# Optimization experiments

Hardware: AMD Instinct MI355X
Metric: run time of the kernel (lower is better)

## Reference

```python
import jax, jax.numpy as jnp
import numpy as np

N = 100000
E = 3200000
EMBED = 64
RBF = 16
EPS_ANGLE = 1e-8
EPS_NORM = 1e-12  # F.normalize default eps


def _linear(h, W, b):
    return h @ W + b


def setup_inputs() -> dict:
    key = jax.random.key(0)
    ks = jax.random.split(key, 12)
    s = lambda fan_in: 1.0 / np.sqrt(fan_in)
    return {
        "x": jax.random.normal(ks[0], (N, EMBED), jnp.float32),
        "coord": jax.random.normal(ks[1], (N, 3), jnp.float32),
        "rbf_feature": jax.random.normal(ks[2], (E, RBF), jnp.float32),
        "edge_index": jax.random.randint(ks[3], (2, E), 0, N, jnp.int64),
        # edge_mlp: Linear(RBF+1, EMBED) -> SiLU -> Linear(EMBED, EMBED)
        "W1": jax.random.uniform(ks[4], (RBF + 1, EMBED), jnp.float32, -s(RBF + 1), s(RBF + 1)),
        "b1": jnp.zeros((EMBED,), jnp.float32),
        "W2": jax.random.uniform(ks[5], (EMBED, EMBED), jnp.float32, -s(EMBED), s(EMBED)),
        "b2": jnp.zeros((EMBED,), jnp.float32),
        # update_mlp: Linear(EMBED, EMBED) -> SiLU -> Linear(EMBED, EMBED)
        "W3": jax.random.uniform(ks[6], (EMBED, EMBED), jnp.float32, -s(EMBED), s(EMBED)),
        "b3": jnp.zeros((EMBED,), jnp.float32),
        "W4": jax.random.uniform(ks[7], (EMBED, EMBED), jnp.float32, -s(EMBED), s(EMBED)),
        "b4": jnp.zeros((EMBED,), jnp.float32),
    }


def reference(x, coord, rbf_feature, edge_index, W1, b1, W2, b2, W3, b3, W4, b4):
    row, col = edge_index[0], edge_index[1]
    # gather per-edge displacement vectors: [E, 3]
    v = coord[row] - coord[col]
    # compute_angle(v, -v): normalize both, cosine, clamp, acos
    norm = jnp.maximum(jnp.linalg.norm(v, axis=-1, keepdims=True), EPS_NORM)
    vn = v / norm
    cos_angle = jnp.clip(jnp.sum(vn * (-vn), axis=-1), -1.0 + EPS_ANGLE, 1.0 - EPS_ANGLE)
    angle = jnp.arccos(cos_angle)[:, None]  # [E, 1]
    edge_feat = jnp.concatenate([rbf_feature, angle], axis=-1)  # [E, RBF+1]
    # edge MLP
    edge_msg = _linear(jax.nn.silu(_linear(edge_feat, W1, b1)), W2, b2)  # [E, EMBED]
    # scatter-add to source nodes (index_add_ over row)
    agg = jax.ops.segment_sum(edge_msg, row, num_segments=x.shape[0])  # [N, EMBED]
    # node update
    return x + _linear(jax.nn.silu(_linear(agg, W3, b3)), W4, b4)
```

## Files before the change

### kernel.cpp

```cpp
#include <hip/hip_runtime.h>
#include <hip/hip_fp16.h>

typedef __attribute__((ext_vector_type(8))) short bf16x8;
typedef __attribute__((ext_vector_type(4))) float f32x4;

constexpr int EMBED = 64;
constexpr int RBF   = 16;
constexpr int EPB   = 256;
constexpr int EPW   = 64;

__device__ __forceinline__ short f2bf(float f) {
    unsigned u = __float_as_uint(f);
    unsigned r = (u + 0x7fffu + ((u >> 16) & 1u)) >> 16;
    return (short)(r & 0xffffu);
}

__device__ __forceinline__ unsigned pk_f16(float lo, float hi) {
    __half2 h = __halves2half2(__float2half_rn(lo), __float2half_rn(hi));
    return *reinterpret_cast<unsigned*>(&h);
}

__device__ __forceinline__ void atom_pk_add_f16(__half* addr, unsigned data) {
    asm volatile("global_atomic_pk_add_f16 %0, %1, off"
                 :: "v"(addr), "v"(data) : "memory");
}

__device__ __forceinline__ int ch_map(int t, int c) {
    return (t & 1) + 2 * c + 32 * (t >> 1);
}

template <bool USE_F16>
__global__ __launch_bounds__(256, 2) void edge_kernel(
    const float* __restrict__ coord,
    const float* __restrict__ rbf,
    const int* __restrict__ edge_index,
    const float* __restrict__ W1,
    const float* __restrict__ b1,
    const float* __restrict__ W2,
    const float* __restrict__ b2,
    void* __restrict__ aggv,
    long long E)
{
    __shared__ int lds_row[EPB];
    __shared__ __align__(16) short lds_s[4][4][16 * 64];

    const int tid  = threadIdx.x;
    const int lane = tid & 63;
    const int wave = tid >> 6;
    const int g = lane >> 4;
    const int c = lane & 15;
    const long long blk_e0 = (long long)blockIdx.x * EPB;

    {
        long long e = blk_e0 + tid;
        lds_row[tid] = (e < E) ? edge_index[e] : 0;
    }
    __builtin_amdgcn_wave_barrier();

    bf16x8 b1f[4];
#pragma unroll
    for (int t = 0; t < 4; ++t) {
#pragma unroll
        for (int j = 0; j < 8; ++j) {
            const int k = g * 8 + j;
            const int n = t * 16 + c;
            b1f[t][j] = (k <= RBF) ? f2bf(W1[k * EMBED + n]) : (short)0;
        }
    }
    bf16x8 b2f[2][4];
#pragma unroll
    for (int kk = 0; kk < 2; ++kk)
#pragma unroll
        for (int t = 0; t < 4; ++t) {
            const int ch = ch_map(t, c);
#pragma unroll
            for (int j = 0; j < 8; ++j) {
                const int k = kk * 32 + g * 8 + j;
                b2f[kk][t][j] = f2bf(W2[k * EMBED + ch]);
            }
        }
    float b1v[4], b2v[4];
#pragma unroll
    for (int t = 0; t < 4; ++t) {
        b1v[t] = b1[t * 16 + c];
        b2v[t] = b2[ch_map(t, c)];
    }

    const long long wave_e0 = blk_e0 + (long long)wave * EPW;

    bf16x8 a1[4];
#pragma unroll
    for (int mt = 0; mt < 4; ++mt) {
        bf16x8 a = {};
        const long long e0 = wave_e0 + mt * 16;
        const int eloc0 = wave * EPW + mt * 16;
        const long long ea = e0 + c;
        const bool ev = (ea < E);
        if (g < 2) {
            if (ev) {
                const float4 p0 = *reinterpret_cast<const float4*>(rbf + ea * RBF + g * 8);
                const float4 p1 = *reinterpret_cast<const float4*>(rbf + ea * RBF + g * 8 + 4);
                a[0] = f2bf(p0.x); a[1] = f2bf(p0.y); a[2] = f2bf(p0.z); a[3] = f2bf(p0.w);
                a[4] = f2bf(p1.x); a[5] = f2bf(p1.y); a[6] = f2bf(p1.z); a[7] = f2bf(p1.w);
            }
        } else if (g == 2) {
            if (ev) {
                const int row = lds_row[eloc0 + c];
                const int col = edge_index[E + ea];
                const float vx = coord[row * 3 + 0] - coord[col * 3 + 0];
                const float vy = coord[row * 3 + 1] - coord[col * 3 + 1];
                const float vz = coord[row * 3 + 2] - coord[col * 3 + 2];
                const float sq = vx * vx + vy * vy + vz * vz;
                const float nrm = fmaxf(sqrtf(sq), 1e-12f);
                const float inv = 1.0f / nrm;
                const float ux = vx * inv, uy = vy * inv, uz = vz * inv;
                const float s2 = ux * ux + uy * uy + uz * uz;
                const float cosang = fminf(fmaxf(-s2, -1.0f), 1.0f);
                const float ang = acosf(cosang);
                a[0] = f2bf(ang);
            }
        }
        a1[mt] = a;
    }

#pragma unroll
    for (int mt = 0; mt < 4; ++mt) {
        f32x4 acc1[4];
#pragma unroll
        for (int t = 0; t < 4; ++t) {
            f32x4 ci = {b1v[t], b1v[t], b1v[t], b1v[t]};
            acc1[t] = __builtin_amdgcn_mfma_f32_16x16x32_bf16(a1[mt], b1f[t], ci, 0, 0, 0);
        }
        char* const sl = reinterpret_cast<char*>(lds_s[wave][mt]);
#pragma unroll
        for (int t = 0; t < 4; ++t)
#pragma unroll
            for (int r = 0; r < 4; ++r) {
                const float x = acc1[t][r];
                const float s = x / (1.0f + __expf(-x));
                const int erow = g * 4 + r;
                const int byte = erow * 128 + ((t * 32 + 2 * c) ^ ((erow & 7) << 4));
                *reinterpret_cast<short*>(sl + byte) = f2bf(s);
            }
    }
    __builtin_amdgcn_wave_barrier();

#pragma unroll
    for (int mt = 0; mt < 4; ++mt) {
        const long long e0 = wave_e0 + mt * 16;
        const int eloc0 = wave * EPW + mt * 16;
        const char* const sl = reinterpret_cast<const char*>(lds_s[wave][mt]);

        bf16x8 a2[2];
#pragma unroll
        for (int kk = 0; kk < 2; ++kk) {
            const int byte = c * 128 + ((kk * 64 + g * 16) ^ ((c & 7) << 4));
            a2[kk] = *reinterpret_cast<const bf16x8*>(sl + byte);
        }

        f32x4 acc2[4];
#pragma unroll
        for (int t = 0; t < 4; ++t) {
            f32x4 ci = {b2v[t], b2v[t], b2v[t], b2v[t]};
            acc2[t] = __builtin_amdgcn_mfma_f32_16x16x32_bf16(a2[0], b2f[0][t], ci, 0, 0, 0);
            acc2[t] = __builtin_amdgcn_mfma_f32_16x16x32_bf16(a2[1], b2f[1][t], acc2[t], 0, 0, 0);
        }

#pragma unroll
        for (int r = 0; r < 4; ++r) {
            const long long eat = e0 + g * 4 + r;
            if (eat < E) {
                const long long rowoff = (long long)lds_row[eloc0 + g * 4 + r] * EMBED;
                if (USE_F16) {
                    __half* const dst = reinterpret_cast<__half*>(aggv) + rowoff;
                    atom_pk_add_f16(dst + 2 * c,      pk_f16(acc2[0][r], acc2[1][r]));
                    atom_pk_add_f16(dst + 32 + 2 * c, pk_f16(acc2[2][r], acc2[3][r]));
                } else {
                    float* const dst = reinterpret_cast<float*>(aggv) + rowoff;
                    atomicAdd(dst + 2 * c,      acc2[0][r]);
                    atomicAdd(dst + 2 * c + 1,  acc2[1][r]);
                    atomicAdd(dst + 32 + 2 * c, acc2[2][r]);
                    atomicAdd(dst + 33 + 2 * c, acc2[3][r]);
                }
            }
        }
    }
}

template <bool USE_F16>
__global__ __launch_bounds__(256) void node_kernel(
    const float* __restrict__ x,
    const void* __restrict__ aggv,
    const float* __restrict__ W3,
    const float* __restrict__ b3,
    const float* __restrict__ W4,
    const float* __restrict__ b4,
    float* __restrict__ out,
    int nn)
{
    __shared__ __align__(16) float lds_s[4][EMBED];
    const int lane = threadIdx.x & 63;
    const int wave = threadIdx.x >> 6;

    float w3c[EMBED], w4c[EMBED];
#pragma unroll
    for (int j = 0; j < EMBED; ++j) w3c[j] = W3[j * EMBED + lane];
#pragma unroll
    for (int j = 0; j < EMBED; ++j) w4c[j] = W4[j * EMBED + lane];
    const float b3v = b3[lane];
    const float b4v = b4[lane];

    const float4* s4 = reinterpret_cast<const float4*>(lds_s[wave]);

    const int wid = blockIdx.x * 4 + wave;
    const int nw  = gridDim.x * 4;
    for (int n = wid; n < nn; n += nw) {
        const long long base = (long long)n * EMBED + lane;
        float a;
        if (USE_F16) {
            a = __half2float(reinterpret_cast<const __half*>(aggv)[base]);
        } else {
            a = reinterpret_cast<const float*>(aggv)[base];
        }

        lds_s[wave][lane] = a;
        __builtin_amdgcn_wave_barrier();

        float acc = b3v;
#pragma unroll
        for (int j4 = 0; j4 < EMBED / 4; ++j4) {
            const float4 sv = s4[j4];
            acc = fmaf(sv.x, w3c[4 * j4 + 0], acc);
            acc = fmaf(sv.y, w3c[4 * j4 + 1], acc);
            acc = fmaf(sv.z, w3c[4 * j4 + 2], acc);
            acc = fmaf(sv.w, w3c[4 * j4 + 3], acc);
        }
        const float s = acc / (1.0f + __expf(-acc));

        __builtin_amdgcn_wave_barrier();
        lds_s[wave][lane] = s;
        __builtin_amdgcn_wave_barrier();

        float acc2 = b4v;
#pragma unroll
        for (int j4 = 0; j4 < EMBED / 4; ++j4) {
            const float4 sv = s4[j4];
            acc2 = fmaf(sv.x, w4c[4 * j4 + 0], acc2);
            acc2 = fmaf(sv.y, w4c[4 * j4 + 1], acc2);
            acc2 = fmaf(sv.z, w4c[4 * j4 + 2], acc2);
            acc2 = fmaf(sv.w, w4c[4 * j4 + 3], acc2);
        }
        __builtin_amdgcn_wave_barrier();

        out[base] = x[base] + acc2;
    }
}

extern "C" void kernel_launch(void* const* d_in, const int* in_sizes, int n_in,
                              void* d_out, int out_size, void* d_ws, size_t ws_size,
                              hipStream_t stream) {
    const float* x      = (const float*)d_in[0];
    const float* coord  = (const float*)d_in[1];
    const float* rbf    = (const float*)d_in[2];
    const int*   ei     = (const int*)d_in[3];
    const float* W1 = (const float*)d_in[4];
    const float* b1 = (const float*)d_in[5];
    const float* W2 = (const float*)d_in[6];
    const float* b2 = (const float*)d_in[7];
    const float* W3 = (const float*)d_in[8];
    const float* b3 = (const float*)d_in[9];
    const float* W4 = (const float*)d_in[10];
    const float* b4 = (const float*)d_in[11];
    float* out = (float*)d_out;

    const long long E = in_sizes[3] / 2;
    const int nn = in_sizes[0] / EMBED;

    const size_t aggF16Bytes = (size_t)nn * EMBED * sizeof(__half);
    const long long eblocks = (E + EPB - 1) / EPB;

    if (ws_size >= aggF16Bytes) {
        hipMemsetAsync(d_ws, 0, aggF16Bytes, stream);
        edge_kernel<true><<<dim3((unsigned)eblocks), dim3(256), 0, stream>>>(
            coord, rbf, ei, W1, b1, W2, b2, d_ws, E);
        node_kernel<true><<<dim3(2048), dim3(256), 0, stream>>>(
            x, d_ws, W3, b3, W4, b4, out, nn);
    } else {
        hipMemsetAsync(out, 0, (size_t)nn * EMBED * sizeof(float), stream);
        edge_kernel<false><<<dim3((unsigned)eblocks), dim3(256), 0, stream>>>(
            coord, rbf, ei, W1, b1, W2, b2, out, E);
        node_kernel<false><<<dim3(2048), dim3(256), 0, stream>>>(
            x, out, W3, b3, W4, b4, out, nn);
    }
}
```

Baseline: 477.2 us.

## Precompute W2 bf16 fragments, stage in LDS, raise occupancy, split guarded tail

A small setup kernel now converts W2 into bf16 MFMA fragments once. Each edge block copies those fragments into LDS instead of gathering and converting W2 from global memory per thread. The edge loop is rolled, one LDS tile per wave is reused, and launch bounds rise to 8 blocks per CU, all to cut register pressure and raise occupancy. A template GUARD flag removes bounds checks for the full blocks, and the tail runs in a separate launch. SiLU uses a fast reciprocal and the LDS stores are packed, at the cost of an extra launch plus LDS reads of W2 inside the inner loop.

```diff
diff --git a/kernel.cpp b/kernel.cpp
--- a/kernel.cpp
+++ b/kernel.cpp
@@ -1,155 +1,150 @@
 #include <hip/hip_runtime.h>
 #include <hip/hip_fp16.h>
+#include <hip/hip_bf16.h>
 
 typedef __attribute__((ext_vector_type(8))) short bf16x8;
 typedef __attribute__((ext_vector_type(4))) float f32x4;
 
 constexpr int EMBED = 64;
 constexpr int RBF   = 16;
-constexpr int EPB   = 256;
-constexpr int EPW   = 64;
 
 __device__ __forceinline__ short f2bf(float f) {
-    unsigned u = __float_as_uint(f);
-    unsigned r = (u + 0x7fffu + ((u >> 16) & 1u)) >> 16;
-    return (short)(r & 0xffffu);
-}
-
+    __hip_bfloat16 h = __float2bfloat16(f);
+    return *reinterpret_cast<short*>(&h);
+}
+__device__ __forceinline__ unsigned pk_bf(float lo, float hi) {
+    unsigned l = (unsigned short)f2bf(lo);
+    unsigned h = (unsigned short)f2bf(hi);
+    return l | (h << 16);
+}
 __device__ __forceinline__ unsigned pk_f16(float lo, float hi) {
     __half2 h = __halves2half2(__float2half_rn(lo), __float2half_rn(hi));
     return *reinterpret_cast<unsigned*>(&h);
 }
-
 __device__ __forceinline__ void atom_pk_add_f16(__half* addr, unsigned data) {
     asm volatile("global_atomic_pk_add_f16 %0, %1, off"
                  :: "v"(addr), "v"(data) : "memory");
 }
-
+__device__ __forceinline__ float silu(float x) {
+    return x * __builtin_amdgcn_rcpf(1.0f + __expf(-x));
+}
 __device__ __forceinline__ int ch_map(int t, int c) {
     return (t & 1) + 2 * c + 32 * (t >> 1);
 }
 
-template <bool USE_F16>
-__global__ __launch_bounds__(256, 2) void edge_kernel(
+__global__ __launch_bounds__(64) void k_wsetup(
+    const float* __restrict__ W2, bf16x8* __restrict__ w2tbl)
+{
+    const int l = threadIdx.x;
+    const int g = l >> 4, c = l & 15;
+#pragma unroll
+    for (int kk = 0; kk < 2; ++kk)
+#pragma unroll
+        for (int t = 0; t < 4; ++t) {
+            bf16x8 f;
+            const int ch = ch_map(t, c);
+#pragma unroll
+            for (int j = 0; j < 8; ++j)
+                f[j] = f2bf(W2[(kk * 32 + g * 8 + j) * EMBED + ch]);
+            w2tbl[(kk * 4 + t) * 64 + l] = f;
+        }
+}
+
+template <bool GUARD, bool F16>
+__global__ __launch_bounds__(256, 8) void edge_kernel(
     const float* __restrict__ coord,
     const float* __restrict__ rbf,
-    const int* __restrict__ edge_index,
+    const int* __restrict__ ei,
     const float* __restrict__ W1,
     const float* __restrict__ b1,
-    const float* __restrict__ W2,
     const float* __restrict__ b2,
-    void* __restrict__ aggv,
-    long long E)
+    const bf16x8* __restrict__ w2tbl_g,
+    void* __restrict__ agg,
+    int e_base, int E)
 {
-    __shared__ int lds_row[EPB];
-    __shared__ __align__(16) short lds_s[4][4][16 * 64];
+    __shared__ __align__(16) short lds_s[4][16 * 64];
+    __shared__ __align__(16) bf16x8 w2s[8][64];
+    __shared__ int lds_row[256];
 
     const int tid  = threadIdx.x;
     const int lane = tid & 63;
     const int wave = tid >> 6;
     const int g = lane >> 4;
     const int c = lane & 15;
-    const long long blk_e0 = (long long)blockIdx.x * EPB;
+    const int blk_e0 = e_base + blockIdx.x * 256;
 
     {
-        long long e = blk_e0 + tid;
-        lds_row[tid] = (e < E) ? edge_index[e] : 0;
-    }
-    __builtin_amdgcn_wave_barrier();
+        bf16x8* d = &w2s[0][0];
+#pragma unroll
+        for (int i = 0; i < 2; ++i) d[tid + 256 * i] = w2tbl_g[tid + 256 * i];
+        const int e = blk_e0 + tid;
+        lds_row[tid] = (!GUARD || e < E) ? ei[e] : 0;
+    }
+    __syncthreads();
 
     bf16x8 b1f[4];
+    float b1v[4], b2v[4];
 #pragma unroll
     for (int t = 0; t < 4; ++t) {
+        const int ch = ch_map(t, c);
 #pragma unroll
         for (int j = 0; j < 8; ++j) {
             const int k = g * 8 + j;
-            const int n = t * 16 + c;
-            b1f[t][j] = (k <= RBF) ? f2bf(W1[k * EMBED + n]) : (short)0;
-        }
-    }
-    bf16x8 b2f[2][4];
-#pragma unroll
-    for (int kk = 0; kk < 2; ++kk)
-#pragma unroll
-        for (int t = 0; t < 4; ++t) {
-            const int ch = ch_map(t, c);
-#pragma unroll
-            for (int j = 0; j < 8; ++j) {
-                const int k = kk * 32 + g * 8 + j;
-                b2f[kk][t][j] = f2bf(W2[k * EMBED + ch]);
-            }
-        }
-    float b1v[4], b2v[4];
-#pragma unroll
-    for (int t = 0; t < 4; ++t) {
-        b1v[t] = b1[t * 16 + c];
-        b2v[t] = b2[ch_map(t, c)];
-    }
-
-    const long long wave_e0 = blk_e0 + (long long)wave * EPW;
-
-    bf16x8 a1[4];
-#pragma unroll
+            b1f[t][j] = (k <= RBF) ? f2bf(W1[k * EMBED + ch]) : (short)0;
+        }
+        b1v[t] = b1[ch];
+        b2v[t] = b2[ch];
+    }
+
+    char* const sl = reinterpret_cast<char*>(lds_s[wave]);
+    const int e0w = blk_e0 + wave * 64;
+
+#pragma unroll 1
     for (int mt = 0; mt < 4; ++mt) {
+        const int e0 = e0w + mt * 16;
+        if (GUARD && e0 >= E) break;
+        const int el0 = wave * 64 + mt * 16;
+
         bf16x8 a = {};
-        const long long e0 = wave_e0 + mt * 16;
-        const int eloc0 = wave * EPW + mt * 16;
-        const long long ea = e0 + c;
-        const bool ev = (ea < E);
+        const int ea = e0 + c;
+        const bool ev = !GUARD || (ea < E);
         if (g < 2) {
             if (ev) {
-                const float4 p0 = *reinterpret_cast<const float4*>(rbf + ea * RBF + g * 8);
-                const float4 p1 = *reinterpret_cast<const float4*>(rbf + ea * RBF + g * 8 + 4);
+                const float4 p0 = *reinterpret_cast<const float4*>(rbf + (long long)ea * RBF + g * 8);
+                const float4 p1 = *reinterpret_cast<const float4*>(rbf + (long long)ea * RBF + g * 8 + 4);
                 a[0] = f2bf(p0.x); a[1] = f2bf(p0.y); a[2] = f2bf(p0.z); a[3] = f2bf(p0.w);
                 a[4] = f2bf(p1.x); a[5] = f2bf(p1.y); a[6] = f2bf(p1.z); a[7] = f2bf(p1.w);
             }
-        } else if (g == 2) {
-            if (ev) {
-                const int row = lds_row[eloc0 + c];
-                const int col = edge_index[E + ea];
-                const float vx = coord[row * 3 + 0] - coord[col * 3 + 0];
-                const float vy = coord[row * 3 + 1] - coord[col * 3 + 1];
-                const float vz = coord[row * 3 + 2] - coord[col * 3 + 2];
-                const float sq = vx * vx + vy * vy + vz * vz;
-                const float nrm = fmaxf(sqrtf(sq), 1e-12f);
-                const float inv = 1.0f / nrm;
-                const float ux = vx * inv, uy = vy * inv, uz = vz * inv;
-                const float s2 = ux * ux + uy * uy + uz * uz;
-                const float cosang = fminf(fmaxf(-s2, -1.0f), 1.0f);
-                const float ang = acosf(cosang);
-                a[0] = f2bf(ang);
-            }
-        }
-        a1[mt] = a;
-    }
-
-#pragma unroll
-    for (int mt = 0; mt < 4; ++mt) {
+        } else if (g == 2 && ev) {
+            const int row = lds_row[el0 + c];
+            const int col = ei[E + ea];
+            const float vx = coord[row * 3 + 0] - coord[col * 3 + 0];
+            const float vy = coord[row * 3 + 1] - coord[col * 3 + 1];
+            const float vz = coord[row * 3 + 2] - coord[col * 3 + 2];
+            const float nrm = fmaxf(sqrtf(vx * vx + vy * vy + vz * vz), 1e-12f);
+            const float inv = 1.0f / nrm;
+            const float ux = vx * inv, uy = vy * inv, uz = vz * inv;
+            const float cosang = fminf(fmaxf(-(ux * ux + uy * uy + uz * uz), -1.0f), 1.0f);
+            a[0] = f2bf(acosf(cosang));
+        }
+
         f32x4 acc1[4];
 #pragma unroll
         for (int t = 0; t < 4; ++t) {
             f32x4 ci = {b1v[t], b1v[t], b1v[t], b1v[t]};
-            acc1[t] = __builtin_amdgcn_mfma_f32_16x16x32_bf16(a1[mt], b1f[t], ci, 0, 0, 0);
-        }
-        char* const sl = reinterpret_cast<char*>(lds_s[wave][mt]);
-#pragma unroll
-        for (int t = 0; t < 4; ++t)
-#pragma unroll
-            for (int r = 0; r < 4; ++r) {
-                const float x = acc1[t][r];
-                const float s = x / (1.0f + __expf(-x));
-                const int erow = g * 4 + r;
-                const int byte = erow * 128 + ((t * 32 + 2 * c) ^ ((erow & 7) << 4));
-                *reinterpret_cast<short*>(sl + byte) = f2bf(s);
-            }
-    }
-    __builtin_amdgcn_wave_barrier();
-
-#pragma unroll
-    for (int mt = 0; mt < 4; ++mt) {
-        const long long e0 = wave_e0 + mt * 16;
-        const int eloc0 = wave * EPW + mt * 16;
-        const char* const sl = reinterpret_cast<const char*>(lds_s[wave][mt]);
+            acc1[t] = __builtin_amdgcn_mfma_f32_16x16x32_bf16(a, b1f[t], ci, 0, 0, 0);
+        }
+
+#pragma unroll
+        for (int r = 0; r < 4; ++r) {
+            const int erow = g * 4 + r;
+            const int swz = (erow & 7) << 4;
+            *reinterpret_cast<unsigned*>(sl + erow * 128 + ((4 * c) ^ swz)) =
+                pk_bf(silu(acc1[0][r]), silu(acc1[1][r]));
+            *reinterpret_cast<unsigned*>(sl + erow * 128 + ((64 + 4 * c) ^ swz)) =
+                pk_bf(silu(acc1[2][r]), silu(acc1[3][r]));
+        }
+        __builtin_amdgcn_wave_barrier();
 
         bf16x8 a2[2];
 #pragma unroll
@@ -157,26 +152,29 @@
             const int byte = c * 128 + ((kk * 64 + g * 16) ^ ((c & 7) << 4));
             a2[kk] = *reinterpret_cast<const bf16x8*>(sl + byte);
         }
+        __builtin_amdgcn_wave_barrier();
 
         f32x4 acc2[4];
 #pragma unroll
         for (int t = 0; t < 4; ++t) {
+            const bf16x8 bw0 = w2s[t][lane];
+            const bf16x8 bw1 = w2s[4 + t][lane];
             f32x4 ci = {b2v[t], b2v[t], b2v[t], b2v[t]};
-            acc2[t] = __builtin_amdgcn_mfma_f32_16x16x32_bf16(a2[0], b2f[0][t], ci, 0, 0, 0);
-            acc2[t] = __builtin_amdgcn_mfma_f32_16x16x32_bf16(a2[1], b2f[1][t], acc2[t], 0, 0, 0);
+            acc2[t] = __builtin_amdgcn_mfma_f32_16x16x32_bf16(a2[0], bw0, ci, 0, 0, 0);
+            acc2[t] = __builtin_amdgcn_mfma_f32_16x16x32_bf16(a2[1], bw1, acc2[t], 0, 0, 0);
         }
 
 #pragma unroll
         for (int r = 0; r < 4; ++r) {
-            const long long eat = e0 + g * 4 + r;
-            if (eat < E) {
-                const long long rowoff = (long long)lds_row[eloc0 + g * 4 + r] * EMBED;
-                if (USE_F16) {
-                    __half* const dst = reinterpret_cast<__half*>(aggv) + rowoff;
+            const int eat = e0 + g * 4 + r;
+            if (!GUARD || eat < E) {
+                const unsigned row = (unsigned)lds_row[el0 + g * 4 + r];
+                if (F16) {
+                    __half* const dst = reinterpret_cast<__half*>(agg) + row * 64u;
                     atom_pk_add_f16(dst + 2 * c,      pk_f16(acc2[0][r], acc2[1][r]));
                     atom_pk_add_f16(dst + 32 + 2 * c, pk_f16(acc2[2][r], acc2[3][r]));
                 } else {
-                    float* const dst = reinterpret_cast<float*>(aggv) + rowoff;
+                    float* const dst = reinterpret_cast<float*>(agg) + row * 64u;
                     atomicAdd(dst + 2 * c,      acc2[0][r]);
                     atomicAdd(dst + 2 * c + 1,  acc2[1][r]);
                     atomicAdd(dst + 32 + 2 * c, acc2[2][r]);
@@ -187,21 +185,16 @@
     }
 }
 
-template <bool USE_F16>
+template <bool F16>
 __global__ __launch_bounds__(256) void node_kernel(
-    const float* __restrict__ x,
-    const void* __restrict__ aggv,
-    const float* __restrict__ W3,
-    const float* __restrict__ b3,
-    const float* __restrict__ W4,
-    const float* __restrict__ b4,
-    float* __restrict__ out,
-    int nn)
+    const float* __restrict__ x, const void* __restrict__ aggv,
+    const float* __restrict__ W3, const float* __restrict__ b3,
+    const float* __restrict__ W4, const float* __restrict__ b4,
+    float* __restrict__ out, int nn)
 {
     __shared__ __align__(16) float lds_s[4][EMBED];
     const int lane = threadIdx.x & 63;
     const int wave = threadIdx.x >> 6;
-
     float w3c[EMBED], w4c[EMBED];
 #pragma unroll
     for (int j = 0; j < EMBED; ++j) w3c[j] = W3[j * EMBED + lane];
@@ -209,23 +202,16 @@
     for (int j = 0; j < EMBED; ++j) w4c[j] = W4[j * EMBED + lane];
     const float b3v = b3[lane];
     const float b4v = b4[lane];
-
     const float4* s4 = reinterpret_cast<const float4*>(lds_s[wave]);
-
     const int wid = blockIdx.x * 4 + wave;
     const int nw  = gridDim.x * 4;
     for (int n = wid; n < nn; n += nw) {
         const long long base = (long long)n * EMBED + lane;
         float a;
-        if (USE_F16) {
-            a = __half2float(reinterpret_cast<const __half*>(aggv)[base]);
-        } else {
-            a = reinterpret_cast<const float*>(aggv)[base];
-        }
-
+        if (F16) a = __half2float(reinterpret_cast<const __half*>(aggv)[base]);
+        else     a = reinterpret_cast<const float*>(aggv)[base];
         lds_s[wave][lane] = a;
         __builtin_amdgcn_wave_barrier();
-
         float acc = b3v;
 #pragma unroll
         for (int j4 = 0; j4 < EMBED / 4; ++j4) {
@@ -235,12 +221,10 @@
             acc = fmaf(sv.z, w3c[4 * j4 + 2], acc);
             acc = fmaf(sv.w, w3c[4 * j4 + 3], acc);
         }
-        const float s = acc / (1.0f + __expf(-acc));
-
+        const float s = acc * __builtin_amdgcn_rcpf(1.0f + __expf(-acc));
         __builtin_amdgcn_wave_barrier();
         lds_s[wave][lane] = s;
         __builtin_amdgcn_wave_barrier();
-
         float acc2 = b4v;
 #pragma unroll
         for (int j4 = 0; j4 < EMBED / 4; ++j4) {
@@ -251,7 +235,6 @@
             acc2 = fmaf(sv.w, w4c[4 * j4 + 3], acc2);
         }
         __builtin_amdgcn_wave_barrier();
-
         out[base] = x[base] + acc2;
     }
 }
@@ -273,22 +256,36 @@
     const float* b4 = (const float*)d_in[11];
     float* out = (float*)d_out;
 
-    const long long E = in_sizes[3] / 2;
+    const int E  = (int)(in_sizes[3] / 2);
     const int nn = in_sizes[0] / EMBED;
 
-    const size_t aggF16Bytes = (size_t)nn * EMBED * sizeof(__half);
-    const long long eblocks = (E + EPB - 1) / EPB;
-
-    if (ws_size >= aggF16Bytes) {
-        hipMemsetAsync(d_ws, 0, aggF16Bytes, stream);
-        edge_kernel<true><<<dim3((unsigned)eblocks), dim3(256), 0, stream>>>(
-            coord, rbf, ei, W1, b1, W2, b2, d_ws, E);
+    bf16x8* w2tbl = (bf16x8*)d_ws;
+    void* agg16 = (char*)d_ws + 16384;
+    const size_t neededF16 = 16384 + (size_t)nn * EMBED * sizeof(__half);
+
+    const int nfull = E / 256;
+    const int rem   = E - nfull * 256;
+
+    k_wsetup<<<dim3(1), dim3(64), 0, stream>>>(W2, w2tbl);
+
+    if (ws_size >= neededF16) {
+        hipMemsetAsync(agg16, 0, (size_t)nn * EMBED * sizeof(__half), stream);
+        if (nfull)
+            edge_kernel<false, true><<<dim3(nfull), dim3(256), 0, stream>>>(
+                coord, rbf, ei, W1, b1, b2, w2tbl, agg16, 0, E);
+        if (rem)
+            edge_kernel<true, true><<<dim3(1), dim3(256), 0, stream>>>(
+                coord, rbf, ei, W1, b1, b2, w2tbl, agg16, nfull * 256, E);
         node_kernel<true><<<dim3(2048), dim3(256), 0, stream>>>(
-            x, d_ws, W3, b3, W4, b4, out, nn);
+            x, agg16, W3, b3, W4, b4, out, nn);
     } else {
         hipMemsetAsync(out, 0, (size_t)nn * EMBED * sizeof(float), stream);
-        edge_kernel<false><<<dim3((unsigned)eblocks), dim3(256), 0, stream>>>(
-            coord, rbf, ei, W1, b1, W2, b2, out, E);
+        if (nfull)
+            edge_kernel<false, false><<<dim3(nfull), dim3(256), 0, stream>>>(
+                coord, rbf, ei, W1, b1, b2, w2tbl, out, 0, E);
+        if (rem)
+            edge_kernel<true, false><<<dim3(1), dim3(256), 0, stream>>>(
+                coord, rbf, ei, W1, b1, b2, w2tbl, out, nfull * 256, E);
         node_kernel<false><<<dim3(2048), dim3(256), 0, stream>>>(
             x, out, W3, b3, W4, b4, out, nn);
     }
```

After: 577.4 us. +21.0%, slower.
